# Performance work log

Hardware: AMD Instinct MI355X
Metric: run time of the kernel (lower is better)

Reference implementation:

```python
import jax, jax.numpy as jnp
import numpy as np

N, E, IN, HID, HEADS, OUT = 50000, 800000, 128, 32, 4, 2
NEG = 0.2   # LeakyReLU negative slope (PyG default)
EPS = 1e-5  # BatchNorm eps


def setup_inputs() -> dict:
    key = jax.random.key(0)
    ks = jax.random.split(key, 32)
    g = lambda i, shape, s=0.05: (jax.random.normal(ks[i], shape, jnp.float32) * s)
    d = {
        'x': jax.random.normal(ks[0], (N, IN), jnp.float32),
        'edge_index': jax.random.randint(ks[1], (2, E), 0, N, jnp.int32),
        'edge_attr': jax.random.normal(ks[2], (E, 1), jnp.float32),
        # conv1: GATv2, in=IN, out=HID, heads=HEADS, edge_dim=1
        'c1_Wl': g(3, (IN, HEADS * HID)), 'c1_bl': g(4, (HEADS * HID,)),
        'c1_Wr': g(5, (IN, HEADS * HID)), 'c1_br': g(6, (HEADS * HID,)),
        'c1_We': g(7, (1, HEADS * HID)),
        'c1_att': g(8, (HEADS, HID)),
        'c1_bias': g(9, (HEADS * HID,)),
        'bn1_gamma': jnp.ones((HEADS * HID,), jnp.float32),
        'bn1_beta': jnp.zeros((HEADS * HID,), jnp.float32),
        'bn1_mean': g(10, (HEADS * HID,)),
        'bn1_var': jax.random.uniform(ks[11], (HEADS * HID,), jnp.float32, 0.5, 1.5),
        # conv2: GATv2, in=HEADS*HID, out=HID, heads=1, edge_dim=1
        'c2_Wl': g(12, (HEADS * HID, HID)), 'c2_bl': g(13, (HID,)),
        'c2_Wr': g(14, (HEADS * HID, HID)), 'c2_br': g(15, (HID,)),
        'c2_We': g(16, (1, HID)),
        'c2_att': g(17, (1, HID)),
        'c2_bias': g(18, (HID,)),
        'bn2_gamma': jnp.ones((HID,), jnp.float32),
        'bn2_beta': jnp.zeros((HID,), jnp.float32),
        'bn2_mean': g(19, (HID,)),
        'bn2_var': jax.random.uniform(ks[20], (HID,), jnp.float32, 0.5, 1.5),
        # classifier
        'clf_W': g(21, (HID, OUT)), 'clf_b': g(22, (OUT,)),
    }
    return d


def _gatv2(x, src, dst, eattr, Wl, bl, Wr, br, We, att, bias, heads, out_ch, concat):
    n = x.shape[0]
    xl = (x @ Wl + bl).reshape(n, heads, out_ch)   # source transform
    xr = (x @ Wr + br).reshape(n, heads, out_ch)   # target transform
    el = (eattr @ We).reshape(-1, heads, out_ch)   # edge transform (no bias in PyG)
    s = xl[src] + xr[dst] + el                     # [E, H, C]
    s = jnp.where(s > 0, s, NEG * s)               # LeakyReLU
    logits = jnp.einsum('ehc,hc->eh', s, att)      # [E, H]
    # segment softmax over destination nodes (every node has a self-loop)
    m = jax.ops.segment_max(logits, dst, num_segments=n)
    a = jnp.exp(logits - m[dst])
    denom = jax.ops.segment_sum(a, dst, num_segments=n)
    alpha = a / denom[dst]                         # [E, H]
    out = jax.ops.segment_sum(alpha[:, :, None] * xl[src], dst, num_segments=n)
    out = out.reshape(n, heads * out_ch) if concat else out.mean(axis=1)
    return out + bias


def _bn_eval(x, gamma, beta, mean, var):
    return (x - mean) * (gamma / jnp.sqrt(var + EPS)) + beta


def reference(x, edge_index, edge_attr,
              c1_Wl, c1_bl, c1_Wr, c1_br, c1_We, c1_att, c1_bias,
              bn1_gamma, bn1_beta, bn1_mean, bn1_var,
              c2_Wl, c2_bl, c2_Wr, c2_br, c2_We, c2_att, c2_bias,
              bn2_gamma, bn2_beta, bn2_mean, bn2_var,
              clf_W, clf_b):
    n = x.shape[0]
    # add self-loops once (PyG GATv2 default add_self_loops=True, fill_value='mean')
    loop = jnp.arange(n, dtype=edge_index.dtype)
    src = jnp.concatenate([edge_index[0], loop])
    dst = jnp.concatenate([edge_index[1], loop])
    loop_attr = jnp.broadcast_to(edge_attr.mean(axis=0, keepdims=True), (n, edge_attr.shape[1]))
    eattr = jnp.concatenate([edge_attr, loop_attr], axis=0)

    h = _gatv2(x, src, dst, eattr, c1_Wl, c1_bl, c1_Wr, c1_br, c1_We, c1_att, c1_bias,
               HEADS, HID, True)
    h = jax.nn.relu(_bn_eval(h, bn1_gamma, bn1_beta, bn1_mean, bn1_var))
    # dropout inactive in eval mode
    h = _gatv2(h, src, dst, eattr, c2_Wl, c2_bl, c2_Wr, c2_br, c2_We, c2_att, c2_bias,
               1, HID, True)
    h = jax.nn.relu(_bn_eval(h, bn2_gamma, bn2_beta, bn2_mean, bn2_var))
    return h @ clf_W + clf_b
```

## Files before the change

kernel.cpp:

```cpp
#include <hip/hip_runtime.h>

#define NNODES 50000
#define NEDGES 800000
#define ETOT   850000
#define IN_CH  128
#define HID    32
#define C1     128
#define NEG    0.2f
#define BNEPS  1e-5f
#define XFB2   1563
#define HB8    391
#define XFEB   1955
#define WTS    160
#define XSS    136
#define NC     16
#define SCB    196
#define FEB    782
#define FLB    49
#define EB1    2048
#define EB2    2048
#define L2E    1.4426950408889634f

#if defined(__has_builtin)
#if __has_builtin(__builtin_amdgcn_exp2f)
#define EXP2F(x) __builtin_amdgcn_exp2f(x)
#endif
#endif
#ifndef EXP2F
#define EXP2F(x) exp2f(x)
#endif

typedef __attribute__((ext_vector_type(8))) short short8;
typedef __attribute__((ext_vector_type(4))) float f32x4;

__device__ __forceinline__ unsigned short bf16r(float f) {
    unsigned u = __float_as_uint(f);
    return (unsigned short)((u + 0x7fffu + ((u >> 16) & 1u)) >> 16);
}
__device__ __forceinline__ unsigned bf16pair(float f0, float f1) {
    return (unsigned)bf16r(f0) | ((unsigned)bf16r(f1) << 16);
}
__device__ __forceinline__ float blo(unsigned u) { return __uint_as_float(u << 16); }
__device__ __forceinline__ float bhi(unsigned u) { return __uint_as_float(u & 0xffff0000u); }

__device__ __forceinline__ int block_iscan(int v, int* ls) {
    int lane = threadIdx.x & 63, w = threadIdx.x >> 6;
    #pragma unroll
    for (int o = 1; o < 64; o <<= 1) {
        int t = __shfl_up(v, o);
        if (lane >= o) v += t;
    }
    if (lane == 63) ls[w] = v;
    __syncthreads();
    int add = 0;
    #pragma unroll
    for (int i = 0; i < 4; i++) add += (i < w) ? ls[i] : 0;
    return v + add;
}

__global__ __launch_bounds__(256) void k_prep(const float* __restrict__ Wl1,
                                              const float* __restrict__ Wr1,
                                              const float* __restrict__ Wl2,
                                              const float* __restrict__ Wr2,
                                              unsigned short* __restrict__ WT,
                                              unsigned short* __restrict__ WT2,
                                              int* __restrict__ hist,
                                              float* __restrict__ meanbuf) {
    int idx = blockIdx.x * 256 + threadIdx.x;
    if (idx == 0) meanbuf[0] = 0.f;
    for (int i = idx; i < NC * NNODES; i += 160 * 256) hist[i] = 0;
    if (idx < 32768) {
        int mat = idx >> 14, rem = idx & 16383;
        int k = rem >> 7, n = rem & 127;
        float v = mat ? Wr1[k * 128 + n] : Wl1[k * 128 + n];
        WT[(size_t)(mat * 128 + n) * WTS + k] = bf16r(v);
    } else {
        int i2 = idx - 32768;
        int mat = i2 >> 12, rem = i2 & 4095;
        int k = rem >> 5, n = rem & 31;
        float v = mat ? Wr2[k * 32 + n] : Wl2[k * 32 + n];
        WT2[(size_t)(mat * 32 + n) * WTS + k] = bf16r(v);
    }
}

__global__ __launch_bounds__(256) void k_xf_eh(
    const float* __restrict__ x,
    const float* __restrict__ bl, const float* __restrict__ br,
    const unsigned short* __restrict__ WT,
    unsigned* __restrict__ xlb, float* __restrict__ xr,
    const int* __restrict__ ei, const float* __restrict__ ea,
    int* __restrict__ hist, int* __restrict__ eoff,
    float* __restrict__ meanbuf) {
    __shared__ short xs_s[64 * XSS];
    int bi = blockIdx.x;
    if (bi % 5 == 0) {
        float* ls = (float*)xs_s;
        int hb = bi / 5;
        int e0 = hb * 2048 + threadIdx.x;
        float v = 0.f;
        if (hb < HB8 - 1) {
            #pragma unroll
            for (int j = 0; j < 8; j++) {
                int e = e0 + 256 * j;
                int c = (8 * hb + j) & (NC - 1);
                eoff[e] = atomicAdd(&hist[c * NNODES + ei[NEDGES + e]], 1);
                v += ea[e];
            }
        } else {
            #pragma unroll
            for (int j = 0; j < 8; j++) {
                int e = e0 + 256 * j;
                if (e < NEDGES) {
                    int c = (8 * hb + j) & (NC - 1);
                    eoff[e] = atomicAdd(&hist[c * NNODES + ei[NEDGES + e]], 1);
                    v += ea[e];
                }
            }
        }
        #pragma unroll
        for (int o = 32; o > 0; o >>= 1) v += __shfl_down(v, o, 64);
        if ((threadIdx.x & 63) == 0) ls[threadIdx.x >> 6] = v;
        __syncthreads();
        if (threadIdx.x == 0) atomicAdd(meanbuf, ls[0] + ls[1] + ls[2] + ls[3]);
        return;
    }
    int g = bi - bi / 5 - 1;
    if (g >= XFB2) return;
    int n0g = g * 32;
    {
        int nd = threadIdx.x >> 3, kc = (threadIdx.x & 7) * 16;
        bool valid = (n0g + nd) < NNODES;
        float xv[16];
        #pragma unroll
        for (int i = 0; i < 4; i++) {
            float4 t = valid ? ((const float4*)(x + (size_t)(n0g + nd) * IN_CH + kc))[i]
                             : make_float4(0.f, 0.f, 0.f, 0.f);
            xv[4 * i] = t.x; xv[4 * i + 1] = t.y; xv[4 * i + 2] = t.z; xv[4 * i + 3] = t.w;
        }
        unsigned hi[8], lo[8];
        #pragma unroll
        for (int i = 0; i < 8; i++) {
            unsigned short h0 = bf16r(xv[2 * i]), h1 = bf16r(xv[2 * i + 1]);
            float l0 = xv[2 * i]     - __uint_as_float(((unsigned)h0) << 16);
            float l1 = xv[2 * i + 1] - __uint_as_float(((unsigned)h1) << 16);
            hi[i] = (unsigned)h0 | ((unsigned)h1 << 16);
            lo[i] = bf16pair(l0, l1);
        }
        uint4* ph = (uint4*)&xs_s[nd * XSS + kc];
        ph[0] = make_uint4(hi[0], hi[1], hi[2], hi[3]);
        ph[1] = make_uint4(hi[4], hi[5], hi[6], hi[7]);
        uint4* pl = (uint4*)&xs_s[(nd + 32) * XSS + kc];
        pl[0] = make_uint4(lo[0], lo[1], lo[2], lo[3]);
        pl[1] = make_uint4(lo[4], lo[5], lo[6], lo[7]);
    }
    __syncthreads();
    int lane = threadIdx.x & 63;
    int lm = lane & 15, q = lane >> 4;
    int w = threadIdx.x >> 6;
    int n0 = w * 64;
    f32x4 acc[2][4];
    #pragma unroll
    for (int mt = 0; mt < 2; mt++)
        #pragma unroll
        for (int nt = 0; nt < 4; nt++) acc[mt][nt] = (f32x4)0.f;

    #pragma unroll
    for (int ks = 0; ks < 4; ks++) {
        int k0 = ks * 32 + q * 8;
        short8 ah0 = *(const short8*)&xs_s[(lm)      * XSS + k0];
        short8 ah1 = *(const short8*)&xs_s[(16 + lm) * XSS + k0];
        short8 al0 = *(const short8*)&xs_s[(32 + lm) * XSS + k0];
        short8 al1 = *(const short8*)&xs_s[(48 + lm) * XSS + k0];
        #pragma unroll
        for (int nt = 0; nt < 4; nt++) {
            short8 bfr = *(const short8*)(WT + (size_t)(n0 + nt * 16 + lm) * WTS + k0);
            acc[0][nt] = __builtin_amdgcn_mfma_f32_16x16x32_bf16(al0, bfr, acc[0][nt], 0, 0, 0);
            acc[0][nt] = __builtin_amdgcn_mfma_f32_16x16x32_bf16(ah0, bfr, acc[0][nt], 0, 0, 0);
            acc[1][nt] = __builtin_amdgcn_mfma_f32_16x16x32_bf16(al1, bfr, acc[1][nt], 0, 0, 0);
            acc[1][nt] = __builtin_amdgcn_mfma_f32_16x16x32_bf16(ah1, bfr, acc[1][nt], 0, 0, 0);
        }
    }
    if (w < 2) {
        #pragma unroll
        for (int nt = 0; nt < 4; nt++) {
            int ch = n0 + nt * 16 + lm;
            float bv = bl[ch];
            #pragma unroll
            for (int mt = 0; mt < 2; mt++)
                #pragma unroll
                for (int r = 0; r < 4; r++) {
                    int node = n0g + mt * 16 + q * 4 + r;
                    float val = acc[mt][nt][r] + bv;
                    float pv = __shfl_xor(val, 1);
                    if ((lm & 1) == 0 && node < NNODES)
                        xlb[(size_t)node * 64 + (ch >> 1)] = bf16pair(val, pv);
                }
        }
    } else {
        #pragma unroll
        for (int nt = 0; nt < 4; nt++) {
            int ch = n0 - 128 + nt * 16 + lm;
            float bv = br[ch];
            #pragma unroll
            for (int mt = 0; mt < 2; mt++)
                #pragma unroll
                for (int r = 0; r < 4; r++) {
                    int node = n0g + mt * 16 + q * 4 + r;
                    if (node < NNODES)
                        xr[(size_t)node * C1 + ch] = acc[mt][nt][r] + bv;
                }
        }
    }
}

__global__ __launch_bounds__(256) void k_red(int* __restrict__ hist,
                                             int* __restrict__ deg,
                                             int* __restrict__ bsum) {
    __shared__ int ls[4];
    int d = blockIdx.x * 256 + threadIdx.x;
    int s = 0;
    if (d < NNODES) {
        #pragma unroll
        for (int c = 0; c < NC; c++) {
            int v = hist[c * NNODES + d];
            hist[c * NNODES + d] = s;
            s += v;
        }
        deg[d] = s;
    }
    int v = (d < NNODES) ? s + 1 : 0;
    #pragma unroll
    for (int o = 32; o > 0; o >>= 1) v += __shfl_down(v, o, 64);
    if ((threadIdx.x & 63) == 0) ls[threadIdx.x >> 6] = v;
    __syncthreads();
    if (threadIdx.x == 0) bsum[blockIdx.x] = ls[0] + ls[1] + ls[2] + ls[3];
}

__global__ __launch_bounds__(256) void k_rowp(const int* __restrict__ deg,
                                              const int* __restrict__ bsum,
                                              int* __restrict__ rowptr) {
    __shared__ int ls[4];
    int t = threadIdx.x;
    int bv = (t < SCB) ? bsum[t] : 0;
    int bincl = block_iscan(bv, ls);
    __shared__ int boffs[256];
    boffs[t] = bincl - bv;
    __syncthreads();
    int base = boffs[blockIdx.x];
    __syncthreads();
    int d = blockIdx.x * 256 + t;
    int v = (d < NNODES) ? deg[d] + 1 : 0;
    int incl = block_iscan(v, ls);
    if (d < NNODES) rowptr[d] = base + incl - v;
    if (d == NNODES - 1) rowptr[NNODES] = base + incl;
}

__global__ __launch_bounds__(256) void k_fill(const int* __restrict__ ei,
                                              const float* __restrict__ ea,
                                              const int* __restrict__ rowptr,
                                              const float* __restrict__ meanbuf,
                                              const int* __restrict__ hist,
                                              const int* __restrict__ eoff,
                                              unsigned* __restrict__ cpack) {
    int blk = blockIdx.x, tid = threadIdx.x;
    if (blk < FEB) {
        int e0 = blk * 1024 + tid;
        int d[4], sv[4], rp[4], hs[4], eo[4];
        float av[4];
        bool ok[4];
        #pragma unroll
        for (int j = 0; j < 4; j++) {
            int e = e0 + 256 * j;
            ok[j] = e < NEDGES;
            int es = ok[j] ? e : 0;
            d[j]  = ei[NEDGES + es];
            sv[j] = ei[es];
            av[j] = ea[es];
            eo[j] = eoff[es];
        }
        #pragma unroll
        for (int j = 0; j < 4; j++) {
            int e = e0 + 256 * j;
            int c = (e >> 8) & (NC - 1);
            rp[j] = rowptr[d[j]];
            hs[j] = hist[c * NNODES + d[j]];
        }
        #pragma unroll
        for (int j = 0; j < 4; j++)
            if (ok[j])
                cpack[rp[j] + 1 + hs[j] + eo[j]] =
                    ((unsigned)bf16r(av[j]) << 16) | (unsigned)sv[j];
        return;
    }
    if (blk < FEB + FLB) {
        float mv = meanbuf[0] * (1.0f / NEDGES);
        unsigned mp = ((unsigned)bf16r(mv)) << 16;
        int i0 = (blk - FEB) * 1024 + tid;
        int rp[4];
        bool ok[4];
        #pragma unroll
        for (int j = 0; j < 4; j++) {
            int i = i0 + 256 * j;
            ok[j] = i < NNODES;
            rp[j] = rowptr[ok[j] ? i : 0];
        }
        #pragma unroll
        for (int j = 0; j < 4; j++)
            if (ok[j]) cpack[rp[j]] = mp | (unsigned)(i0 + 256 * j);
        return;
    }
    if (tid < 64) cpack[ETOT + tid] = 0u;
}

__global__ __launch_bounds__(256) void k_edge1(
    const unsigned* __restrict__ xlb, const float* __restrict__ xr,
    const int* __restrict__ rowptr, const unsigned* __restrict__ cpack,
    const float* __restrict__ We, const float* __restrict__ att,
    float* __restrict__ out1) {
    int lane = threadIdx.x & 63;
    int q = lane & 15, s = lane >> 4;
    int node = blockIdx.x * 4 + (threadIdx.x >> 6);
    if (node >= NNODES) return;
    const int W = EB1 * 4;
    const float C6 = 0.6f * L2E, C4 = 0.4f * L2E;
    float4 we0 = ((const float4*)We)[2 * q],  we1 = ((const float4*)We)[2 * q + 1];
    float4 av0 = ((const float4*)att)[2 * q], av1 = ((const float4*)att)[2 * q + 1];
    float4 aA0 = make_float4(av0.x * C6, av0.y * C6, av0.z * C6, av0.w * C6);
    float4 aB0 = make_float4(av0.x * C4, av0.y * C4, av0.z * C4, av0.w * C4);
    float4 aA1 = make_float4(av1.x * C6, av1.y * C6, av1.z * C6, av1.w * C6);
    float4 aB1 = make_float4(av1.x * C4, av1.y * C4, av1.z * C4, av1.w * C4);
    const uint4* xlv = (const uint4*)xlb;
    int r0 = rowptr[node], r1 = rowptr[node + 1];
    float4 xr0 = ((const float4*)xr)[(size_t)node * 32 + 2 * q];
    float4 xr1 = ((const float4*)xr)[(size_t)node * 32 + 2 * q + 1];
    for (;;) {
        int nn = node + W;
        bool more = nn < NNODES;
        int nr0 = 0, nr1 = 0;
        float4 nxr0 = make_float4(0.f, 0.f, 0.f, 0.f);
        float4 nxr1 = make_float4(0.f, 0.f, 0.f, 0.f);
        if (more) {
            nr0 = rowptr[nn]; nr1 = rowptr[nn + 1];
            nxr0 = ((const float4*)xr)[(size_t)nn * 32 + 2 * q];
            nxr1 = ((const float4*)xr)[(size_t)nn * 32 + 2 * q + 1];
        }
        float den = 0.f;
        float a0 = 0.f, a1 = 0.f, a2 = 0.f, a3 = 0.f;
        float a4 = 0.f, a5 = 0.f, a6 = 0.f, a7 = 0.f;
        int nit = (r1 - r0 + 3) >> 2;
        int k = r0 + s;
        unsigned sc0 = cpack[k];
        unsigned sc1 = cpack[k + 4];
        unsigned sc2 = cpack[k + 8];
        unsigned sc3 = cpack[k + 12];
        unsigned sc4 = cpack[k + 16];
        uint4 xv0 = xlv[(size_t)(sc0 & 0xffffu) * 16 + q];
        uint4 xv1 = xlv[(size_t)(sc1 & 0xffffu) * 16 + q];
        uint4 xv2 = xlv[(size_t)(sc2 & 0xffffu) * 16 + q];
        for (int it = 0; it < nit; it++) {
            unsigned scn = cpack[k + 20];
            uint4 xvn = xlv[(size_t)(sc3 & 0xffffu) * 16 + q];
            bool ok = k < r1;
            float av = __uint_as_float(sc0 & 0xffff0000u);
            float x0 = blo(xv0.x), x1 = bhi(xv0.x), x2 = blo(xv0.y), x3 = bhi(xv0.y);
            float x4 = blo(xv0.z), x5 = bhi(xv0.z), x6 = blo(xv0.w), x7 = bhi(xv0.w);
            float s0 = fmaf(av, we0.x, x0 + xr0.x);
            float s1 = fmaf(av, we0.y, x1 + xr0.y);
            float s2 = fmaf(av, we0.z, x2 + xr0.z);
            float s3 = fmaf(av, we0.w, x3 + xr0.w);
            float s4 = fmaf(av, we1.x, x4 + xr1.x);
            float s5 = fmaf(av, we1.y, x5 + xr1.y);
            float s6 = fmaf(av, we1.z, x6 + xr1.z);
            float s7 = fmaf(av, we1.w, x7 + xr1.w);
            float tA = s0 * aA0.x;            tA = fmaf(fabsf(s0), aB0.x, tA);
            tA = fmaf(s1, aA0.y, tA);         tA = fmaf(fabsf(s1), aB0.y, tA);
            tA = fmaf(s2, aA0.z, tA);         tA = fmaf(fabsf(s2), aB0.z, tA);
            tA = fmaf(s3, aA0.w, tA);         tA = fmaf(fabsf(s3), aB0.w, tA);
            float tB = s4 * aA1.x;            tB = fmaf(fabsf(s4), aB1.x, tB);
            tB = fmaf(s5, aA1.y, tB);         tB = fmaf(fabsf(s5), aB1.y, tB);
            tB = fmaf(s6, aA1.z, tB);         tB = fmaf(fabsf(s6), aB1.z, tB);
            tB = fmaf(s7, aA1.w, tB);         tB = fmaf(fabsf(s7), aB1.w, tB);
            float t = tA + tB;
            t += __shfl_xor(t, 1);
            t += __shfl_xor(t, 2);
            float e = ok ? EXP2F(t) : 0.f;
            den += e;
            a0 = fmaf(e, x0, a0); a1 = fmaf(e, x1, a1);
            a2 = fmaf(e, x2, a2); a3 = fmaf(e, x3, a3);
            a4 = fmaf(e, x4, a4); a5 = fmaf(e, x5, a5);
            a6 = fmaf(e, x6, a6); a7 = fmaf(e, x7, a7);
            k += 4;
            sc0 = sc1; sc1 = sc2; sc2 = sc3; sc3 = sc4; sc4 = scn;
            xv0 = xv1; xv1 = xv2; xv2 = xvn;
        }
        #pragma unroll
        for (int o = 16; o <= 32; o <<= 1) {
            den += __shfl_xor(den, o);
            a0 += __shfl_xor(a0, o); a1 += __shfl_xor(a1, o);
            a2 += __shfl_xor(a2, o); a3 += __shfl_xor(a3, o);
            a4 += __shfl_xor(a4, o); a5 += __shfl_xor(a5, o);
            a6 += __shfl_xor(a6, o); a7 += __shfl_xor(a7, o);
        }
        if (s == 0) {
            float rd = 1.f / den;
            ((float4*)out1)[(size_t)node * 32 + 2 * q] =
                make_float4(a0 * rd, a1 * rd, a2 * rd, a3 * rd);
            ((float4*)out1)[(size_t)node * 32 + 2 * q + 1] =
                make_float4(a4 * rd, a5 * rd, a6 * rd, a7 * rd);
        }
        if (!more) return;
        node = nn; r0 = nr0; r1 = nr1; xr0 = nxr0; xr1 = nxr1;
    }
}

__global__ __launch_bounds__(256) void k_epi(
    const float* __restrict__ out1, const float* __restrict__ bias1,
    const float* __restrict__ g1, const float* __restrict__ b1,
    const float* __restrict__ m1, const float* __restrict__ v1,
    const unsigned short* __restrict__ WT2,
    const float* __restrict__ bl2, const float* __restrict__ br2,
    unsigned* __restrict__ xlb2, float* __restrict__ xr2) {
    __shared__ short hs_s[64 * XSS];
    __shared__ float A[128], B[128];
    int n0g = blockIdx.x * 32;
    if (threadIdx.x < 128) {
        int c = threadIdx.x;
        float sc = g1[c] * rsqrtf(v1[c] + BNEPS);
        A[c] = sc;
        B[c] = (bias1[c] - m1[c]) * sc + b1[c];
    }
    __syncthreads();
    {
        int nd = threadIdx.x >> 3, kc = (threadIdx.x & 7) * 16;
        bool valid = (n0g + nd) < NNODES;
        float xv[16];
        #pragma unroll
        for (int i = 0; i < 4; i++) {
            float4 t = valid ? ((const float4*)(out1 + (size_t)(n0g + nd) * C1 + kc))[i]
                             : make_float4(0.f, 0.f, 0.f, 0.f);
            xv[4 * i] = t.x; xv[4 * i + 1] = t.y; xv[4 * i + 2] = t.z; xv[4 * i + 3] = t.w;
        }
        #pragma unroll
        for (int j = 0; j < 16; j++)
            xv[j] = fmaxf(xv[j] * A[kc + j] + B[kc + j], 0.f);
        unsigned hi[8], lo[8];
        #pragma unroll
        for (int i = 0; i < 8; i++) {
            unsigned short h0 = bf16r(xv[2 * i]), h1 = bf16r(xv[2 * i + 1]);
            float l0 = xv[2 * i]     - __uint_as_float(((unsigned)h0) << 16);
            float l1 = xv[2 * i + 1] - __uint_as_float(((unsigned)h1) << 16);
            hi[i] = (unsigned)h0 | ((unsigned)h1 << 16);
            lo[i] = bf16pair(l0, l1);
        }
        uint4* ph = (uint4*)&hs_s[nd * XSS + kc];
        ph[0] = make_uint4(hi[0], hi[1], hi[2], hi[3]);
        ph[1] = make_uint4(hi[4], hi[5], hi[6], hi[7]);
        uint4* pl = (uint4*)&hs_s[(nd + 32) * XSS + kc];
        pl[0] = make_uint4(lo[0], lo[1], lo[2], lo[3]);
        pl[1] = make_uint4(lo[4], lo[5], lo[6], lo[7]);
    }
    __syncthreads();
    int lane = threadIdx.x & 63;
    int lm = lane & 15, q = lane >> 4;
    int w = threadIdx.x >> 6;
    f32x4 acc[2];
    acc[0] = (f32x4)0.f; acc[1] = (f32x4)0.f;
    #pragma unroll
    for (int ks = 0; ks < 4; ks++) {
        int k0 = ks * 32 + q * 8;
        short8 ah0 = *(const short8*)&hs_s[(lm)      * XSS + k0];
        short8 ah1 = *(const short8*)&hs_s[(16 + lm) * XSS + k0];
        short8 al0 = *(const short8*)&hs_s[(32 + lm) * XSS + k0];
        short8 al1 = *(const short8*)&hs_s[(48 + lm) * XSS + k0];
        short8 bfr = *(const short8*)(WT2 + (size_t)(w * 16 + lm) * WTS + k0);
        acc[0] = __builtin_amdgcn_mfma_f32_16x16x32_bf16(al0, bfr, acc[0], 0, 0, 0);
        acc[0] = __builtin_amdgcn_mfma_f32_16x16x32_bf16(ah0, bfr, acc[0], 0, 0, 0);
        acc[1] = __builtin_amdgcn_mfma_f32_16x16x32_bf16(al1, bfr, acc[1], 0, 0, 0);
        acc[1] = __builtin_amdgcn_mfma_f32_16x16x32_bf16(ah1, bfr, acc[1], 0, 0, 0);
    }
    if (w < 2) {
        int ch = w * 16 + lm;
        float bv = bl2[ch];
        #pragma unroll
        for (int mt = 0; mt < 2; mt++)
            #pragma unroll
            for (int r = 0; r < 4; r++) {
                int node = n0g + mt * 16 + q * 4 + r;
                float val = acc[mt][r] + bv;
                float pv = __shfl_xor(val, 1);
                if ((lm & 1) == 0 && node < NNODES)
                    xlb2[(size_t)node * 16 + (ch >> 1)] = bf16pair(val, pv);
            }
    } else {
        int ch = (w - 2) * 16 + lm;
        float bv = br2[ch];
        #pragma unroll
        for (int mt = 0; mt < 2; mt++)
            #pragma unroll
            for (int r = 0; r < 4; r++) {
                int node = n0g + mt * 16 + q * 4 + r;
                if (node < NNODES)
                    xr2[(size_t)node * HID + ch] = acc[mt][r] + bv;
            }
    }
}

__global__ __launch_bounds__(256) void k_edge2(
    const unsigned* __restrict__ xlb2, const float* __restrict__ xr2,
    const int* __restrict__ rowptr, const unsigned* __restrict__ cpack,
    const float* __restrict__ We2, const float* __restrict__ att2,
    const float* __restrict__ bias2,
    const float* __restrict__ g2, const float* __restrict__ b2,
    const float* __restrict__ m2, const float* __restrict__ v2,
    const float* __restrict__ W, const float* __restrict__ b,
    float* __restrict__ y) {
    int lane = threadIdx.x & 63;
    int q = lane & 7, s = lane >> 3;
    int node = blockIdx.x * 4 + (threadIdx.x >> 6);
    if (node >= NNODES) return;
    const int WV = EB2 * 4;
    const float C6 = 0.6f * L2E, C4 = 0.4f * L2E;
    float4 we = ((const float4*)We2)[q];
    float4 av4 = ((const float4*)att2)[q];
    float4 aA = make_float4(av4.x * C6, av4.y * C6, av4.z * C6, av4.w * C6);
    float4 aB = make_float4(av4.x * C4, av4.y * C4, av4.z * C4, av4.w * C4);
    float4 gv = ((const float4*)g2)[q];
    float4 bv = ((const float4*)b2)[q];
    float4 mv = ((const float4*)m2)[q];
    float4 vv = ((const float4*)v2)[q];
    float4 bi = ((const float4*)bias2)[q];
    float4 sA, sB;
    sA.x = gv.x * rsqrtf(vv.x + BNEPS); sB.x = (bi.x - mv.x) * sA.x + bv.x;
    sA.y = gv.y * rsqrtf(vv.y + BNEPS); sB.y = (bi.y - mv.y) * sA.y + bv.y;
    sA.z = gv.z * rsqrtf(vv.z + BNEPS); sB.z = (bi.z - mv.z) * sA.z + bv.z;
    sA.w = gv.w * rsqrtf(vv.w + BNEPS); sB.w = (bi.w - mv.w) * sA.w + bv.w;
    float4 w0 = ((const float4*)W)[2 * q];
    float4 w1 = ((const float4*)W)[2 * q + 1];
    float bb0 = b[0], bb1 = b[1];
    const uint2* xlv = (const uint2*)xlb2;
    int r0 = rowptr[node], r1 = rowptr[node + 1];
    float4 xr0 = ((const float4*)xr2)[(size_t)node * 8 + q];
    for (;;) {
        int nn = node + WV;
        bool more = nn < NNODES;
        int nr0 = 0, nr1 = 0;
        float4 nxr0 = make_float4(0.f, 0.f, 0.f, 0.f);
        if (more) {
            nr0 = rowptr[nn]; nr1 = rowptr[nn + 1];
            nxr0 = ((const float4*)xr2)[(size_t)nn * 8 + q];
        }
        float den = 0.f;
        float a0 = 0.f, a1 = 0.f, a2 = 0.f, a3 = 0.f;
        int nit = (r1 - r0 + 7) >> 3;
        int k = r0 + s;
        unsigned sc0 = cpack[k];
        unsigned sc1 = cpack[k + 8];
        unsigned sc2 = cpack[k + 16];
        unsigned sc3 = cpack[k + 24];
        unsigned sc4 = cpack[k + 32];
        uint2 xv0 = xlv[(size_t)(sc0 & 0xffffu) * 8 + q];
        uint2 xv1 = xlv[(size_t)(sc1 & 0xffffu) * 8 + q];
        uint2 xv2 = xlv[(size_t)(sc2 & 0xffffu) * 8 + q];
        for (int it = 0; it < nit; it++) {
            unsigned scn = cpack[k + 40];
            uint2 xvn = xlv[(size_t)(sc3 & 0xffffu) * 8 + q];
            bool ok = k < r1;
            float av = __uint_as_float(sc0 & 0xffff0000u);
            float x0 = blo(xv0.x), x1 = bhi(xv0.x), x2 = blo(xv0.y), x3 = bhi(xv0.y);
            float s0 = fmaf(av, we.x, x0 + xr0.x);
            float s1 = fmaf(av, we.y, x1 + xr0.y);
            float s2 = fmaf(av, we.z, x2 + xr0.z);
            float s3 = fmaf(av, we.w, x3 + xr0.w);
            float tA = s0 * aA.x;             tA = fmaf(fabsf(s0), aB.x, tA);
            tA = fmaf(s1, aA.y, tA);          tA = fmaf(fabsf(s1), aB.y, tA);
            float tB = s2 * aA.z;             tB = fmaf(fabsf(s2), aB.z, tB);
            tB = fmaf(s3, aA.w, tB);          tB = fmaf(fabsf(s3), aB.w, tB);
            float t = tA + tB;
            t += __shfl_xor(t, 1);
            t += __shfl_xor(t, 2);
            t += __shfl_xor(t, 4);
            float e = ok ? EXP2F(t) : 0.f;
            den += e;
            a0 = fmaf(e, x0, a0); a1 = fmaf(e, x1, a1);
            a2 = fmaf(e, x2, a2); a3 = fmaf(e, x3, a3);
            k += 8;
            sc0 = sc1; sc1 = sc2; sc2 = sc3; sc3 = sc4; sc4 = scn;
            xv0 = xv1; xv1 = xv2; xv2 = xvn;
        }
        #pragma unroll
        for (int o = 8; o <= 32; o <<= 1) {
            den += __shfl_xor(den, o);
            a0 += __shfl_xor(a0, o); a1 += __shfl_xor(a1, o);
            a2 += __shfl_xor(a2, o); a3 += __shfl_xor(a3, o);
        }
        float rd = 1.f / den;
        float h0 = fmaxf(fmaf(a0 * rd, sA.x, sB.x), 0.f);
        float h1 = fmaxf(fmaf(a1 * rd, sA.y, sB.y), 0.f);
        float h2 = fmaxf(fmaf(a2 * rd, sA.z, sB.z), 0.f);
        float h3 = fmaxf(fmaf(a3 * rd, sA.w, sB.w), 0.f);
        float u0 = h0 * w0.x + h1 * w0.z + h2 * w1.x + h3 * w1.z;
        float u1 = h0 * w0.y + h1 * w0.w + h2 * w1.y + h3 * w1.w;
        u0 += __shfl_xor(u0, 1); u0 += __shfl_xor(u0, 2); u0 += __shfl_xor(u0, 4);
        u1 += __shfl_xor(u1, 1); u1 += __shfl_xor(u1, 2); u1 += __shfl_xor(u1, 4);
        if (lane == 0) {
            y[(size_t)node * 2]     = u0 + bb0;
            y[(size_t)node * 2 + 1] = u1 + bb1;
        }
        if (!more) return;
        node = nn; r0 = nr0; r1 = nr1; xr0 = nxr0;
    }
}

extern "C" void kernel_launch(void* const* d_in, const int* in_sizes, int n_in,
                              void* d_out, int out_size, void* d_ws, size_t ws_size,
                              hipStream_t stream) {
    const float* x       = (const float*)d_in[0];
    const int*   ei      = (const int*)d_in[1];
    const float* ea      = (const float*)d_in[2];
    const float* c1_Wl   = (const float*)d_in[3];
    const float* c1_bl   = (const float*)d_in[4];
    const float* c1_Wr   = (const float*)d_in[5];
    const float* c1_br   = (const float*)d_in[6];
    const float* c1_We   = (const float*)d_in[7];
    const float* c1_att  = (const float*)d_in[8];
    const float* c1_bias = (const float*)d_in[9];
    const float* bn1_g   = (const float*)d_in[10];
    const float* bn1_b   = (const float*)d_in[11];
    const float* bn1_m   = (const float*)d_in[12];
    const float* bn1_v   = (const float*)d_in[13];
    const float* c2_Wl   = (const float*)d_in[14];
    const float* c2_bl   = (const float*)d_in[15];
    const float* c2_Wr   = (const float*)d_in[16];
    const float* c2_br   = (const float*)d_in[17];
    const float* c2_We   = (const float*)d_in[18];
    const float* c2_att  = (const float*)d_in[19];
    const float* c2_bias = (const float*)d_in[20];
    const float* bn2_g   = (const float*)d_in[21];
    const float* bn2_b   = (const float*)d_in[22];
    const float* bn2_m   = (const float*)d_in[23];
    const float* bn2_v   = (const float*)d_in[24];
    const float* clf_W   = (const float*)d_in[25];
    const float* clf_b   = (const float*)d_in[26];

    float* ws = (float*)d_ws;
    size_t off = 0;
    unsigned* XLb  = (unsigned*)(ws + off); off += (size_t)NNODES * 64;
    float*    XR1  = ws + off; off += (size_t)NNODES * C1;
    float*    OUT1 = ws + off; off += (size_t)NNODES * C1;
    unsigned* XLb2 = (unsigned*)(ws + off); off += (size_t)NNODES * 16;
    float*    XR2  = ws + off; off += (size_t)NNODES * HID;
    unsigned* CPACK= (unsigned*)(ws + off); off += (size_t)ETOT + 64;
    unsigned short* WT  = (unsigned short*)(ws + off); off += 256 * WTS / 2;
    unsigned short* WT2 = (unsigned short*)(ws + off); off += 64 * WTS / 2;
    int*      EOFF = (int*)(ws + off); off += NEDGES;
    int*      ROWP = (int*)(ws + off); off += NNODES + 16;
    int*      DEG  = (int*)(ws + off); off += NNODES;
    int*      BSUM = (int*)(ws + off); off += 256;
    int*      HIST = (int*)(ws + off); off += (size_t)NC * NNODES;
    float*    MEANB= ws + off; off += 64;
    if (ws_size < off * sizeof(float)) return;

    k_prep  <<<160, 256, 0, stream>>>(c1_Wl, c1_Wr, c2_Wl, c2_Wr, WT, WT2, HIST, MEANB);
    k_xf_eh <<<XFEB, 256, 0, stream>>>(x, c1_bl, c1_br, WT, XLb, XR1,
                                       ei, ea, HIST, EOFF, MEANB);
    k_red   <<<SCB, 256, 0, stream>>>(HIST, DEG, BSUM);
    k_rowp  <<<SCB, 256, 0, stream>>>(DEG, BSUM, ROWP);
    k_fill  <<<FEB + FLB + 1, 256, 0, stream>>>(ei, ea, ROWP, MEANB, HIST, EOFF, CPACK);
    k_edge1 <<<EB1, 256, 0, stream>>>(XLb, XR1, ROWP, CPACK, c1_We, c1_att, OUT1);
    k_epi   <<<XFB2, 256, 0, stream>>>(OUT1, c1_bias, bn1_g, bn1_b, bn1_m, bn1_v,
                                       WT2, c2_bl, c2_br, XLb2, XR2);
    k_edge2 <<<EB2, 256, 0, stream>>>(XLb2, XR2, ROWP, CPACK, c2_We, c2_att,
                                      c2_bias, bn2_g, bn2_b, bn2_m, bn2_v,
                                      clf_W, clf_b, (float*)d_out);
}
```

Before: 295.9 us.

## Fuse BN1+ReLU and conv2 linear transform into edge1 aggregation epilogue

Removes the separate k_epi kernel and the OUT1 intermediate buffer. Each wave in k_edge1 now applies the BatchNorm/ReLU affine to its aggregated 128-channel row and multiplies it by a swizzled bf16 copy of the conv2 Wl/Wr weights held in LDS. The per-row matvec is reduced across lanes with a butterfly shuffle before writing xlb2/xr2. The BN scale and shift are precomputed in k_prep. This saves a 25MB write/read round trip and one launch, but swaps MFMA for scalar FMAs with the weights in plain bf16 (the old path used hi/lo split activations), and it adds LDS use and shuffle overhead to the edge kernel.

```diff
diff --git a/kernel.cpp b/kernel.cpp
--- a/kernel.cpp
+++ b/kernel.cpp
@@ -43,6 +43,17 @@
 __device__ __forceinline__ float blo(unsigned u) { return __uint_as_float(u << 16); }
 __device__ __forceinline__ float bhi(unsigned u) { return __uint_as_float(u & 0xffff0000u); }
 
+__device__ __forceinline__ float4 shfl_xor4(float4 v, int m) {
+    return make_float4(__shfl_xor(v.x, m), __shfl_xor(v.y, m),
+                       __shfl_xor(v.z, m), __shfl_xor(v.w, m));
+}
+__device__ __forceinline__ float4 sel4(bool c, float4 a, float4 b) {
+    return make_float4(c ? a.x : b.x, c ? a.y : b.y, c ? a.z : b.z, c ? a.w : b.w);
+}
+__device__ __forceinline__ float4 add4(float4 a, float4 b) {
+    return make_float4(a.x + b.x, a.y + b.y, a.z + b.z, a.w + b.w);
+}
+
 __device__ __forceinline__ int block_iscan(int v, int* ls) {
     int lane = threadIdx.x & 63, w = threadIdx.x >> 6;
     #pragma unroll
@@ -62,12 +73,25 @@
                                               const float* __restrict__ Wr1,
                                               const float* __restrict__ Wl2,
                                               const float* __restrict__ Wr2,
+                                              const float* __restrict__ bias1,
+                                              const float* __restrict__ g1,
+                                              const float* __restrict__ b1,
+                                              const float* __restrict__ m1,
+                                              const float* __restrict__ v1,
                                               unsigned short* __restrict__ WT,
-                                              unsigned short* __restrict__ WT2,
+                                              unsigned short* __restrict__ WC,
+                                              float* __restrict__ A1,
+                                              float* __restrict__ B1,
                                               int* __restrict__ hist,
                                               float* __restrict__ meanbuf) {
     int idx = blockIdx.x * 256 + threadIdx.x;
     if (idx == 0) meanbuf[0] = 0.f;
+    if (blockIdx.x == 0 && threadIdx.x < 128) {
+        int c = threadIdx.x;
+        float sc = g1[c] * rsqrtf(v1[c] + BNEPS);
+        A1[c] = sc;
+        B1[c] = (bias1[c] - m1[c]) * sc + b1[c];
+    }
     for (int i = idx; i < NC * NNODES; i += 160 * 256) hist[i] = 0;
     if (idx < 32768) {
         int mat = idx >> 14, rem = idx & 16383;
@@ -79,7 +103,9 @@
         int mat = i2 >> 12, rem = i2 & 4095;
         int k = rem >> 5, n = rem & 31;
         float v = mat ? Wr2[k * 32 + n] : Wl2[k * 32 + n];
-        WT2[(size_t)(mat * 32 + n) * WTS + k] = bf16r(v);
+        int c = mat * 32 + n;
+        int phys = (c >> 3) ^ ((k >> 3) & 7);
+        WC[k * 64 + (c & 7) + 8 * phys] = bf16r(v);
     }
 }
 
@@ -316,11 +342,21 @@
     const unsigned* __restrict__ xlb, const float* __restrict__ xr,
     const int* __restrict__ rowptr, const unsigned* __restrict__ cpack,
     const float* __restrict__ We, const float* __restrict__ att,
-    float* __restrict__ out1) {
+    const float* __restrict__ A1, const float* __restrict__ B1,
+    const unsigned short* __restrict__ WC,
+    const float* __restrict__ bl2, const float* __restrict__ br2,
+    unsigned* __restrict__ xlb2, float* __restrict__ xr2) {
+    __shared__ unsigned short Wlds[8192];
+    {
+        uint4* dst = (uint4*)Wlds;
+        const uint4* src = (const uint4*)WC;
+        #pragma unroll
+        for (int i = 0; i < 4; i++) dst[threadIdx.x + 256 * i] = src[threadIdx.x + 256 * i];
+    }
+    __syncthreads();
     int lane = threadIdx.x & 63;
     int q = lane & 15, s = lane >> 4;
     int node = blockIdx.x * 4 + (threadIdx.x >> 6);
-    if (node >= NNODES) return;
     const int W = EB1 * 4;
     const float C6 = 0.6f * L2E, C4 = 0.4f * L2E;
     float4 we0 = ((const float4*)We)[2 * q],  we1 = ((const float4*)We)[2 * q + 1];
@@ -329,6 +365,11 @@
     float4 aB0 = make_float4(av0.x * C4, av0.y * C4, av0.z * C4, av0.w * C4);
     float4 aA1 = make_float4(av1.x * C6, av1.y * C6, av1.z * C6, av1.w * C6);
     float4 aB1 = make_float4(av1.x * C4, av1.y * C4, av1.z * C4, av1.w * C4);
+    float4 A80 = ((const float4*)A1)[2 * q], A81 = ((const float4*)A1)[2 * q + 1];
+    float4 B80 = ((const float4*)B1)[2 * q], B81 = ((const float4*)B1)[2 * q + 1];
+    int brev = ((q & 1) << 3) | ((q & 2) << 1) | ((q & 4) >> 1) | ((q & 8) >> 3);
+    int ocol = 16 * s + brev;
+    float bcv = (s < 2) ? bl2[ocol] : br2[ocol - 32];
     const uint4* xlv = (const uint4*)xlb;
     int r0 = rowptr[node], r1 = rowptr[node + 1];
     float4 xr0 = ((const float4*)xr)[(size_t)node * 32 + 2 * q];
@@ -401,107 +442,54 @@
             a4 += __shfl_xor(a4, o); a5 += __shfl_xor(a5, o);
             a6 += __shfl_xor(a6, o); a7 += __shfl_xor(a7, o);
         }
-        if (s == 0) {
-            float rd = 1.f / den;
-            ((float4*)out1)[(size_t)node * 32 + 2 * q] =
-                make_float4(a0 * rd, a1 * rd, a2 * rd, a3 * rd);
-            ((float4*)out1)[(size_t)node * 32 + 2 * q + 1] =
-                make_float4(a4 * rd, a5 * rd, a6 * rd, a7 * rd);
+        float rd = 1.f / den;
+        float h[8];
+        h[0] = fmaxf(fmaf(a0 * rd, A80.x, B80.x), 0.f);
+        h[1] = fmaxf(fmaf(a1 * rd, A80.y, B80.y), 0.f);
+        h[2] = fmaxf(fmaf(a2 * rd, A80.z, B80.z), 0.f);
+        h[3] = fmaxf(fmaf(a3 * rd, A80.w, B80.w), 0.f);
+        h[4] = fmaxf(fmaf(a4 * rd, A81.x, B81.x), 0.f);
+        h[5] = fmaxf(fmaf(a5 * rd, A81.y, B81.y), 0.f);
+        h[6] = fmaxf(fmaf(a6 * rd, A81.z, B81.z), 0.f);
+        h[7] = fmaxf(fmaf(a7 * rd, A81.w, B81.w), 0.f);
+        float4 pA = make_float4(0.f, 0.f, 0.f, 0.f), pB = pA, pC = pA, pD = pA;
+        #pragma unroll
+        for (int j = 0; j < 8; j++) {
+            int row = 8 * q + j;
+            int ph0 = (2 * s) ^ (q & 7);
+            uint4 w0 = ((const uint4*)Wlds)[row * 8 + ph0];
+            uint4 w1 = ((const uint4*)Wlds)[row * 8 + (ph0 ^ 1)];
+            float hj = h[j];
+            pA.x = fmaf(hj, blo(w0.x), pA.x); pA.y = fmaf(hj, bhi(w0.x), pA.y);
+            pA.z = fmaf(hj, blo(w0.y), pA.z); pA.w = fmaf(hj, bhi(w0.y), pA.w);
+            pB.x = fmaf(hj, blo(w0.z), pB.x); pB.y = fmaf(hj, bhi(w0.z), pB.y);
+            pB.z = fmaf(hj, blo(w0.w), pB.z); pB.w = fmaf(hj, bhi(w0.w), pB.w);
+            pC.x = fmaf(hj, blo(w1.x), pC.x); pC.y = fmaf(hj, bhi(w1.x), pC.y);
+            pC.z = fmaf(hj, blo(w1.y), pC.z); pC.w = fmaf(hj, bhi(w1.y), pC.w);
+            pD.x = fmaf(hj, blo(w1.z), pD.x); pD.y = fmaf(hj, bhi(w1.z), pD.y);
+            pD.z = fmaf(hj, blo(w1.w), pD.z); pD.w = fmaf(hj, bhi(w1.w), pD.w);
+        }
+        float4 kA = sel4(q & 1, pC, pA), kB = sel4(q & 1, pD, pB);
+        float4 sA_ = sel4(q & 1, pA, pC), sB_ = sel4(q & 1, pB, pD);
+        kA = add4(kA, shfl_xor4(sA_, 1)); kB = add4(kB, shfl_xor4(sB_, 1));
+        float4 k2 = sel4(q & 2, kB, kA);
+        float4 s2_ = sel4(q & 2, kA, kB);
+        k2 = add4(k2, shfl_xor4(s2_, 2));
+        float v0 = (q & 4) ? k2.z : k2.x, v1 = (q & 4) ? k2.w : k2.y;
+        float u0 = (q & 4) ? k2.x : k2.z, u1 = (q & 4) ? k2.y : k2.w;
+        v0 += __shfl_xor(u0, 4); v1 += __shfl_xor(u1, 4);
+        float vf = (q & 8) ? v1 : v0;
+        float uf = (q & 8) ? v0 : v1;
+        float val = vf + __shfl_xor(uf, 8) + bcv;
+        if (s < 2) {
+            float pv = __shfl_xor(val, 8);
+            if ((q & 8) == 0)
+                xlb2[(size_t)node * 16 + (ocol >> 1)] = bf16pair(val, pv);
+        } else {
+            xr2[(size_t)node * HID + (ocol - 32)] = val;
         }
         if (!more) return;
         node = nn; r0 = nr0; r1 = nr1; xr0 = nxr0; xr1 = nxr1;
-    }
-}
-
-__global__ __launch_bounds__(256) void k_epi(
-    const float* __restrict__ out1, const float* __restrict__ bias1,
-    const float* __restrict__ g1, const float* __restrict__ b1,
-    const float* __restrict__ m1, const float* __restrict__ v1,
-    const unsigned short* __restrict__ WT2,
-    const float* __restrict__ bl2, const float* __restrict__ br2,
-    unsigned* __restrict__ xlb2, float* __restrict__ xr2) {
-    __shared__ short hs_s[64 * XSS];
-    __shared__ float A[128], B[128];
-    int n0g = blockIdx.x * 32;
-    if (threadIdx.x < 128) {
-        int c = threadIdx.x;
-        float sc = g1[c] * rsqrtf(v1[c] + BNEPS);
-        A[c] = sc;
-        B[c] = (bias1[c] - m1[c]) * sc + b1[c];
-    }
-    __syncthreads();
-    {
-        int nd = threadIdx.x >> 3, kc = (threadIdx.x & 7) * 16;
-        bool valid = (n0g + nd) < NNODES;
-        float xv[16];
-        #pragma unroll
-        for (int i = 0; i < 4; i++) {
-            float4 t = valid ? ((const float4*)(out1 + (size_t)(n0g + nd) * C1 + kc))[i]
-                             : make_float4(0.f, 0.f, 0.f, 0.f);
-            xv[4 * i] = t.x; xv[4 * i + 1] = t.y; xv[4 * i + 2] = t.z; xv[4 * i + 3] = t.w;
-        }
-        #pragma unroll
-        for (int j = 0; j < 16; j++)
-            xv[j] = fmaxf(xv[j] * A[kc + j] + B[kc + j], 0.f);
-        unsigned hi[8], lo[8];
-        #pragma unroll
-        for (int i = 0; i < 8; i++) {
-            unsigned short h0 = bf16r(xv[2 * i]), h1 = bf16r(xv[2 * i + 1]);
-            float l0 = xv[2 * i]     - __uint_as_float(((unsigned)h0) << 16);
-            float l1 = xv[2 * i + 1] - __uint_as_float(((unsigned)h1) << 16);
-            hi[i] = (unsigned)h0 | ((unsigned)h1 << 16);
-            lo[i] = bf16pair(l0, l1);
-        }
-        uint4* ph = (uint4*)&hs_s[nd * XSS + kc];
-        ph[0] = make_uint4(hi[0], hi[1], hi[2], hi[3]);
-        ph[1] = make_uint4(hi[4], hi[5], hi[6], hi[7]);
-        uint4* pl = (uint4*)&hs_s[(nd + 32) * XSS + kc];
-        pl[0] = make_uint4(lo[0], lo[1], lo[2], lo[3]);
-        pl[1] = make_uint4(lo[4], lo[5], lo[6], lo[7]);
-    }
-    __syncthreads();
-    int lane = threadIdx.x & 63;
-    int lm = lane & 15, q = lane >> 4;
-    int w = threadIdx.x >> 6;
-    f32x4 acc[2];
-    acc[0] = (f32x4)0.f; acc[1] = (f32x4)0.f;
-    #pragma unroll
-    for (int ks = 0; ks < 4; ks++) {
-        int k0 = ks * 32 + q * 8;
-        short8 ah0 = *(const short8*)&hs_s[(lm)      * XSS + k0];
-        short8 ah1 = *(const short8*)&hs_s[(16 + lm) * XSS + k0];
-        short8 al0 = *(const short8*)&hs_s[(32 + lm) * XSS + k0];
-        short8 al1 = *(const short8*)&hs_s[(48 + lm) * XSS + k0];
-        short8 bfr = *(const short8*)(WT2 + (size_t)(w * 16 + lm) * WTS + k0);
-        acc[0] = __builtin_amdgcn_mfma_f32_16x16x32_bf16(al0, bfr, acc[0], 0, 0, 0);
-        acc[0] = __builtin_amdgcn_mfma_f32_16x16x32_bf16(ah0, bfr, acc[0], 0, 0, 0);
-        acc[1] = __builtin_amdgcn_mfma_f32_16x16x32_bf16(al1, bfr, acc[1], 0, 0, 0);
-        acc[1] = __builtin_amdgcn_mfma_f32_16x16x32_bf16(ah1, bfr, acc[1], 0, 0, 0);
-    }
-    if (w < 2) {
-        int ch = w * 16 + lm;
-        float bv = bl2[ch];
-        #pragma unroll
-        for (int mt = 0; mt < 2; mt++)
-            #pragma unroll
-            for (int r = 0; r < 4; r++) {
-                int node = n0g + mt * 16 + q * 4 + r;
-                float val = acc[mt][r] + bv;
-                float pv = __shfl_xor(val, 1);
-                if ((lm & 1) == 0 && node < NNODES)
-                    xlb2[(size_t)node * 16 + (ch >> 1)] = bf16pair(val, pv);
-            }
-    } else {
-        int ch = (w - 2) * 16 + lm;
-        float bv = br2[ch];
-        #pragma unroll
-        for (int mt = 0; mt < 2; mt++)
-            #pragma unroll
-            for (int r = 0; r < 4; r++) {
-                int node = n0g + mt * 16 + q * 4 + r;
-                if (node < NNODES)
-                    xr2[(size_t)node * HID + ch] = acc[mt][r] + bv;
-            }
     }
 }
 
@@ -646,12 +634,13 @@
     size_t off = 0;
     unsigned* XLb  = (unsigned*)(ws + off); off += (size_t)NNODES * 64;
     float*    XR1  = ws + off; off += (size_t)NNODES * C1;
-    float*    OUT1 = ws + off; off += (size_t)NNODES * C1;
     unsigned* XLb2 = (unsigned*)(ws + off); off += (size_t)NNODES * 16;
     float*    XR2  = ws + off; off += (size_t)NNODES * HID;
     unsigned* CPACK= (unsigned*)(ws + off); off += (size_t)ETOT + 64;
-    unsigned short* WT  = (unsigned short*)(ws + off); off += 256 * WTS / 2;
-    unsigned short* WT2 = (unsigned short*)(ws + off); off += 64 * WTS / 2;
+    unsigned short* WT = (unsigned short*)(ws + off); off += 256 * WTS / 2;
+    unsigned short* WC = (unsigned short*)(ws + off); off += 4096;
+    float*    A1v  = ws + off; off += 128;
+    float*    B1v  = ws + off; off += 128;
     int*      EOFF = (int*)(ws + off); off += NEDGES;
     int*      ROWP = (int*)(ws + off); off += NNODES + 16;
     int*      DEG  = (int*)(ws + off); off += NNODES;
@@ -660,15 +649,16 @@
     float*    MEANB= ws + off; off += 64;
     if (ws_size < off * sizeof(float)) return;
 
-    k_prep  <<<160, 256, 0, stream>>>(c1_Wl, c1_Wr, c2_Wl, c2_Wr, WT, WT2, HIST, MEANB);
+    k_prep  <<<160, 256, 0, stream>>>(c1_Wl, c1_Wr, c2_Wl, c2_Wr,
+                                      c1_bias, bn1_g, bn1_b, bn1_m, bn1_v,
+                                      WT, WC, A1v, B1v, HIST, MEANB);
     k_xf_eh <<<XFEB, 256, 0, stream>>>(x, c1_bl, c1_br, WT, XLb, XR1,
                                        ei, ea, HIST, EOFF, MEANB);
     k_red   <<<SCB, 256, 0, stream>>>(HIST, DEG, BSUM);
     k_rowp  <<<SCB, 256, 0, stream>>>(DEG, BSUM, ROWP);
     k_fill  <<<FEB + FLB + 1, 256, 0, stream>>>(ei, ea, ROWP, MEANB, HIST, EOFF, CPACK);
-    k_edge1 <<<EB1, 256, 0, stream>>>(XLb, XR1, ROWP, CPACK, c1_We, c1_att, OUT1);
-    k_epi   <<<XFB2, 256, 0, stream>>>(OUT1, c1_bias, bn1_g, bn1_b, bn1_m, bn1_v,
-                                       WT2, c2_bl, c2_br, XLb2, XR2);
+    k_edge1 <<<EB1, 256, 0, stream>>>(XLb, XR1, ROWP, CPACK, c1_We, c1_att,
+                                      A1v, B1v, WC, c2_bl, c2_br, XLb2, XR2);
     k_edge2 <<<EB2, 256, 0, stream>>>(XLb2, XR2, ROWP, CPACK, c2_We, c2_att,
                                       c2_bias, bn2_g, bn2_b, bn2_m, bn2_v,
                                       clf_W, clf_b, (float*)d_out);
```

After: 343.7 us. 1.16x slower.
